# Optimization experiments

Hardware: AMD Instinct MI355X
Metric: run time of the kernel (lower is better)

Reference implementation:

```python
import math
import jax, jax.numpy as jnp
import numpy as np

B_SZ, N_TOK, D_INNER, S_STATE = 4, 1024, 384, 16
DT_MAX = 0.15


def setup_inputs() -> dict:
    key = jax.random.key(0)
    ks = jax.random.split(key, 10)
    dt_init = math.log(math.exp(0.1) - 1.0)  # softplus^-1(0.1)
    x = jax.random.normal(ks[0], (B_SZ, N_TOK, D_INNER), dtype=jnp.float32)
    dt_self_W = jax.random.uniform(ks[1], (D_INNER, D_INNER), minval=-1e-4, maxval=1e-4)
    dt_self_b = jnp.full((D_INNER,), dt_init, dtype=jnp.float32)
    dt_diff_W = jax.random.uniform(ks[2], (D_INNER, D_INNER), minval=-1e-4, maxval=1e-4)
    dt_diff_b = jnp.full((D_INNER,), dt_init, dtype=jnp.float32)
    B_W = jax.random.normal(ks[3], (D_INNER, S_STATE)) / math.sqrt(D_INNER)
    C_real_W = jax.random.normal(ks[4], (D_INNER, S_STATE)) / math.sqrt(D_INNER)
    C_imag_W = jax.random.normal(ks[5], (D_INNER, S_STATE)) / math.sqrt(D_INNER)
    D_param = jnp.ones((D_INNER,), dtype=jnp.float32)
    A_log = jnp.broadcast_to(jnp.log(jnp.arange(1, S_STATE + 1, dtype=jnp.float32))[None, :], (D_INNER, S_STATE))
    lap = jnp.array([[0.0, 1.0, 0.0], [1.0, -4.0, 1.0], [0.0, 1.0, 0.0]], dtype=jnp.float32) * 0.1
    conv_w = jnp.broadcast_to(lap[None, None], (D_INNER, 1, 3, 3)) + 0.01 * jax.random.normal(ks[6], (D_INNER, 1, 3, 3))
    reaction_alpha = 0.01 * jax.random.normal(ks[7], (1, 1, D_INNER, 1))
    reaction_beta = 0.01 * jax.random.normal(ks[8], (1, 1, D_INNER, 1))
    return {
        'x': x, 'dt_self_W': dt_self_W, 'dt_self_b': dt_self_b,
        'dt_diff_W': dt_diff_W, 'dt_diff_b': dt_diff_b,
        'B_W': B_W, 'C_real_W': C_real_W, 'C_imag_W': C_imag_W,
        'D_param': D_param, 'A_log': A_log, 'conv_w': conv_w,
        'reaction_alpha': reaction_alpha, 'reaction_beta': reaction_beta,
        'K_steps': 2,
    }


def _laplacian(h, conv_w, H, W):
    # h: (B, N, D, S) -> depthwise 3x3 conv with replicate pad over the HxW grid
    B, N, D, S = h.shape
    hs = h.transpose(0, 3, 2, 1).reshape(B * S, D, H, W)
    hp = jnp.pad(hs, ((0, 0), (0, 0), (1, 1), (1, 1)), mode='edge')
    lap = jax.lax.conv_general_dilated(
        hp, conv_w, window_strides=(1, 1), padding='VALID',
        feature_group_count=D, dimension_numbers=('NCHW', 'OIHW', 'NCHW'))
    return lap.reshape(B, S, D, N).transpose(0, 3, 2, 1)


def reference(x, dt_self_W, dt_self_b, dt_diff_W, dt_diff_b, B_W, C_real_W,
              C_imag_W, D_param, A_log, conv_w, reaction_alpha, reaction_beta,
              K_steps):
    B, N, D = x.shape
    H = Wg = int(math.sqrt(N))
    A = -jax.nn.softplus(A_log)  # (D, S)
    delta_s = jnp.minimum(jax.nn.softplus(x @ dt_self_W.T + dt_self_b), DT_MAX)[..., None]
    delta_d = jnp.minimum(jax.nn.softplus(x @ dt_diff_W.T + dt_diff_b), DT_MAX)[..., None]
    B_mat = x @ B_W          # (B, N, S)
    C_real = x @ C_real_W    # (B, N, S)
    C_imag = x @ C_imag_W    # (B, N, S)
    mamba_input = jnp.einsum('bnd,bns->bnds', x, B_mat)
    h_real = mamba_input
    h_imag = jnp.zeros_like(h_real)
    dt = 1.0 / K_steps
    A_exp = A[None, None]  # (1,1,D,S)
    for _ in range(K_steps):
        f1_real = delta_s * (A_exp * h_real + mamba_input)
        f1_imag = delta_s * (A_exp * h_imag)
        lap_real = _laplacian(h_real, conv_w, H, Wg)
        lap_imag = _laplacian(h_imag, conv_w, H, Wg)
        f2_real = delta_d * -lap_imag
        f2_imag = delta_d * lap_real
        reaction_scale = reaction_alpha - reaction_beta * (h_real ** 2 + h_imag ** 2)
        h_real = h_real + dt * (f1_real + f2_real + h_real * reaction_scale)
        h_imag = h_imag + dt * (f1_imag + f2_imag + h_imag * reaction_scale)
    y = (jnp.einsum('bnds,bns->bnd', h_real, C_real)
         + jnp.einsum('bnds,bns->bnd', h_imag, C_imag)
         + x * D_param)
    return y
```

## Files before the change

kernel.cpp:

```cpp
#include <hip/hip_runtime.h>
#include <math.h>

#define B_SZ    4
#define N_TOKC  1024
#define D_INNER 384
#define S_STATE 16
#define DT_MAX_V 0.15f
#define PLANE   (B_SZ * N_TOKC)
#define DN      ((size_t)B_SZ * D_INNER * N_TOKC)

typedef __attribute__((ext_vector_type(8))) short bf16x8;
typedef __attribute__((ext_vector_type(4))) float f32x4;

__device__ __forceinline__ float softplusf(float z) {
    return fmaxf(z, 0.f) + log1pf(expf(-fabsf(z)));
}

__device__ __forceinline__ unsigned short f2bf(float f) {
    unsigned u = __float_as_uint(f);
    unsigned r = (u + 0x7FFFu + ((u >> 16) & 1u)) >> 16;
    return (unsigned short)r;
}

__device__ __forceinline__ unsigned packbf(float hr, float hi) {
    return (__float_as_uint(hr) & 0xFFFF0000u) | (__float_as_uint(hi) >> 16);
}

__device__ __forceinline__ size_t frag_off(int T, int kb, int q, int l16) {
    return ((size_t)((T * 12 + kb) * 4 + q)) * 128 + l16 * 8;
}

__device__ __forceinline__ bf16x8 pack8(const float* v) {
    bf16x8 o;
#pragma unroll
    for (int e = 0; e < 8; e++) o[e] = (short)f2bf(v[e]);
    return o;
}

__global__ __launch_bounds__(256) void k_prep(
    const float* __restrict__ x, const float* __restrict__ Ws, const float* __restrict__ Wd,
    const float* __restrict__ BW, const float* __restrict__ CrW, const float* __restrict__ CiW,
    float* __restrict__ x_t, unsigned short* __restrict__ xp,
    unsigned short* __restrict__ Wdtp, unsigned short* __restrict__ Wbcp)
{
    const int t = threadIdx.x;
    const int bx = blockIdx.x;
    if (bx < 1536) {
        __shared__ __align__(16) float tile[32][36];
        const int tok0 = (bx & 127) * 32;
        const int d0   = (bx >> 7) * 32;
        const int b = tok0 >> 10, n0 = tok0 & 1023;
        {
            const int r = t >> 3, c4 = (t & 7) * 4;
            const float4 v = *(const float4*)(x + (size_t)(tok0 + r) * D_INNER + d0 + c4);
            tile[r][c4 + 0] = v.x; tile[r][c4 + 1] = v.y;
            tile[r][c4 + 2] = v.z; tile[r][c4 + 3] = v.w;
        }
        __syncthreads();
        {
            const int dr = t >> 3, n4 = (t & 7) * 4;
            float4 o;
            o.x = tile[n4 + 0][dr]; o.y = tile[n4 + 1][dr];
            o.z = tile[n4 + 2][dr]; o.w = tile[n4 + 3][dr];
            *(float4*)(x_t + ((size_t)(b * D_INNER + d0 + dr)) * N_TOKC + n0 + n4) = o;
        }
        if (t < 128) {
            const int tt = t >> 6, q = (t >> 4) & 3, l16 = t & 15;
            const int row = tt * 16 + l16;
            float v[8];
#pragma unroll
            for (int e = 0; e < 8; e++) v[e] = tile[row][q * 8 + e];
            *(bf16x8*)(xp + frag_off((tok0 >> 4) + tt, d0 >> 5, q, l16)) = pack8(v);
        }
    } else if (bx < 1584) {
        const int vv = bx - 1536;
        const int mat = vv >= 24;
        const int dt16 = mat ? vv - 24 : vv;
        const float* W = mat ? Wd : Ws;
        unsigned short* dst = Wdtp + (size_t)mat * 147456;
#pragma unroll
        for (int it = 0; it < 3; it++) {
            const int item = t + it * 256;
            const int l16 = item & 15, q = (item >> 4) & 3, kb = item >> 6;
            const float* src = W + (size_t)(dt16 * 16 + l16) * D_INNER + kb * 32 + q * 8;
            float v[8];
            const float4 v0 = *(const float4*)(src);
            const float4 v1 = *(const float4*)(src + 4);
            v[0] = v0.x; v[1] = v0.y; v[2] = v0.z; v[3] = v0.w;
            v[4] = v1.x; v[5] = v1.y; v[6] = v1.z; v[7] = v1.w;
            *(bf16x8*)(dst + frag_off(dt16, kb, q, l16)) = pack8(v);
        }
    } else {
        const int m = bx - 1584;
        const float* W2 = (m == 0) ? BW : ((m == 1) ? CrW : CiW);
#pragma unroll
        for (int it = 0; it < 3; it++) {
            const int item = t + it * 256;
            const int l16 = item & 15, q = (item >> 4) & 3, kb = item >> 6;
            float v[8];
#pragma unroll
            for (int e = 0; e < 8; e++)
                v[e] = W2[(size_t)(kb * 32 + q * 8 + e) * S_STATE + l16];
            *(bf16x8*)(Wbcp + (size_t)m * 6144 + frag_off(0, kb, q, l16)) = pack8(v);
        }
    }
}

__global__ __launch_bounds__(256) void k_gemm(
    const unsigned short* __restrict__ xp, const unsigned short* __restrict__ Wdtp,
    const unsigned short* __restrict__ Wbcp,
    const float* __restrict__ bs, const float* __restrict__ bd,
    float* __restrict__ ds_t, float* __restrict__ dd_t,
    float* __restrict__ Bm_t, float* __restrict__ Cr_t, float* __restrict__ Ci_t)
{
    const int wave = threadIdx.x >> 6;
    const int lane = threadIdx.x & 63;
    const int quad = lane >> 4, l16 = lane & 15;

    if (blockIdx.x < 384) {
        const int dbase = (blockIdx.x >> 6) * 64;
        const int tbase = (blockIdx.x & 63) * 64;
        const int wd = (wave & 1) * 32;
        const int wt = (wave >> 1) * 32;
        const int dT0 = (dbase + wd) >> 4;
        const int tT0 = (tbase + wt) >> 4;

        f32x4 acc[2][2][2];
#pragma unroll
        for (int m = 0; m < 2; m++)
#pragma unroll
            for (int i = 0; i < 2; i++)
#pragma unroll
                for (int j = 0; j < 2; j++) acc[m][i][j] = (f32x4)0.f;

#pragma unroll
        for (int kb = 0; kb < 12; kb++) {
            bf16x8 a[2][2], b[2];
#pragma unroll
            for (int m = 0; m < 2; m++)
#pragma unroll
                for (int i = 0; i < 2; i++)
                    a[m][i] = *(const bf16x8*)(Wdtp + (size_t)m * 147456
                                               + frag_off(dT0 + i, kb, quad, l16));
#pragma unroll
            for (int j = 0; j < 2; j++)
                b[j] = *(const bf16x8*)(xp + frag_off(tT0 + j, kb, quad, l16));
#pragma unroll
            for (int m = 0; m < 2; m++)
#pragma unroll
                for (int i = 0; i < 2; i++)
#pragma unroll
                    for (int j = 0; j < 2; j++)
                        acc[m][i][j] = __builtin_amdgcn_mfma_f32_16x16x32_bf16(
                            a[m][i], b[j], acc[m][i][j], 0, 0, 0);
        }

#pragma unroll
        for (int m = 0; m < 2; m++) {
            const float* bias = (m == 0) ? bs : bd;
            float* out = (m == 0) ? ds_t : dd_t;
#pragma unroll
            for (int i = 0; i < 2; i++)
#pragma unroll
                for (int j = 0; j < 2; j++) {
                    const int tok = tbase + wt + j * 16 + l16;
                    const int bb = tok >> 10, n = tok & 1023;
#pragma unroll
                    for (int reg = 0; reg < 4; reg++) {
                        const int d = dbase + wd + i * 16 + quad * 4 + reg;
                        const float v = fminf(softplusf(acc[m][i][j][reg] + bias[d]), DT_MAX_V);
                        out[((size_t)(bb * D_INNER + d)) * N_TOKC + n] = v;
                    }
                }
        }
    } else {
        const int tT = (blockIdx.x - 384) * 4 + wave;
        f32x4 acc[3];
#pragma unroll
        for (int m = 0; m < 3; m++) acc[m] = (f32x4)0.f;

#pragma unroll
        for (int kb = 0; kb < 12; kb++) {
            const bf16x8 b = *(const bf16x8*)(xp + frag_off(tT, kb, quad, l16));
#pragma unroll
            for (int m = 0; m < 3; m++) {
                const bf16x8 a = *(const bf16x8*)(Wbcp + (size_t)m * 6144
                                                  + frag_off(0, kb, quad, l16));
                acc[m] = __builtin_amdgcn_mfma_f32_16x16x32_bf16(a, b, acc[m], 0, 0, 0);
            }
        }

        const int tok = tT * 16 + l16;
#pragma unroll
        for (int m = 0; m < 3; m++) {
            float* plane = (m == 0) ? Bm_t : ((m == 1) ? Cr_t : Ci_t);
#pragma unroll
            for (int reg = 0; reg < 4; reg++) {
                const int s = quad * 4 + reg;
                plane[(size_t)s * PLANE + tok] = acc[m][reg];
            }
        }
    }
}

__global__ __launch_bounds__(256) void k_ssm(
    const float* __restrict__ x_t, const float* __restrict__ conv_w, const float* __restrict__ A_log,
    const float* __restrict__ ralpha, const float* __restrict__ rbeta, const float* __restrict__ Dp,
    const float* __restrict__ ds_t, const float* __restrict__ dd_t,
    const float* __restrict__ Bm_t, const float* __restrict__ Cr_t, const float* __restrict__ Ci_t,
    float* __restrict__ y_part)
{
    const int sg = blockIdx.x;
    const int d  = blockIdx.y;
    const int b  = blockIdx.z;
    const int t  = threadIdx.x;
    const int c  = t & 31;
    const int g  = t >> 5;
    const int r0 = g * 4;

    __shared__ unsigned pl[4][34 * 34];

    float w[9];
#pragma unroll
    for (int i = 0; i < 9; i++) w[i] = conv_w[d * 9 + i];
    const float alpha = ralpha[d];
    const float beta  = rbeta[d];
    const float Dv    = Dp[d];
    float A[4];
#pragma unroll
    for (int s = 0; s < 4; s++) A[s] = -softplusf(A_log[d * S_STATE + sg * 4 + s]);

    const size_t base_dn = ((size_t)(b * D_INNER + d)) * N_TOKC;
    const size_t base_sn = (size_t)b * N_TOKC;

    float xv[4], dsv[4], ddv[4], Bmv[4][4];
    float hr[4][4], hi[4][4];
#pragma unroll
    for (int k = 0; k < 4; k++) {
        const int n = (r0 + k) * 32 + c;
        xv[k]  = x_t [base_dn + n];
        dsv[k] = ds_t[base_dn + n];
        ddv[k] = dd_t[base_dn + n];
#pragma unroll
        for (int s = 0; s < 4; s++) {
            Bmv[k][s] = Bm_t[(size_t)(sg * 4 + s) * PLANE + base_sn + n];
            hr[k][s]  = xv[k] * Bmv[k][s];
        }
    }

    const int wslot = (r0 + 1) * 34 + (c + 1);
    const int rbase = r0 * 34 + c;

#pragma unroll
    for (int s = 0; s < 4; s++) {
#pragma unroll
        for (int k = 0; k < 4; k++)
            pl[s][wslot + k * 34] = __float_as_uint(hr[k][s]);
        if (g == 0) pl[s][c + 1]           = __float_as_uint(hr[0][s]);
        if (g == 7) pl[s][33 * 34 + c + 1] = __float_as_uint(hr[3][s]);
        if (c == 0) {
#pragma unroll
            for (int k = 0; k < 4; k++) pl[s][(r0 + 1 + k) * 34] = __float_as_uint(hr[k][s]);
            if (g == 0) pl[s][0]       = __float_as_uint(hr[0][s]);
            if (g == 7) pl[s][33 * 34] = __float_as_uint(hr[3][s]);
        }
        if (c == 31) {
#pragma unroll
            for (int k = 0; k < 4; k++) pl[s][(r0 + 1 + k) * 34 + 33] = __float_as_uint(hr[k][s]);
            if (g == 0) pl[s][33]           = __float_as_uint(hr[0][s]);
            if (g == 7) pl[s][33 * 34 + 33] = __float_as_uint(hr[3][s]);
        }
    }
    __syncthreads();

    float lr0[4][4];
#pragma unroll
    for (int s = 0; s < 4; s++) {
        float fr[6][3];
#pragma unroll
        for (int rr = 0; rr < 6; rr++)
#pragma unroll
            for (int bb = 0; bb < 3; bb++)
                fr[rr][bb] = __uint_as_float(pl[s][rbase + rr * 34 + bb]);
#pragma unroll
        for (int k = 0; k < 4; k++) {
            float ar = 0.f;
#pragma unroll
            for (int a = 0; a < 3; a++)
#pragma unroll
                for (int bb = 0; bb < 3; bb++)
                    ar = fmaf(w[a * 3 + bb], fr[k + a][bb], ar);
            lr0[k][s] = ar;
        }
    }
    __syncthreads();

#pragma unroll
    for (int k = 0; k < 4; k++)
#pragma unroll
        for (int s = 0; s < 4; s++) {
            const float hrv = hr[k][s];
            const float u   = xv[k] * Bmv[k][s];
            const float f1r = dsv[k] * fmaf(A[s], hrv, u);
            const float rs  = fmaf(-beta, hrv * hrv, alpha);
            hr[k][s] = hrv + 0.5f * (f1r + hrv * rs);
            hi[k][s] = 0.5f * ddv[k] * lr0[k][s];
        }

#pragma unroll
    for (int s = 0; s < 4; s++) {
#pragma unroll
        for (int k = 0; k < 4; k++)
            pl[s][wslot + k * 34] = packbf(hr[k][s], hi[k][s]);
        if (g == 0) pl[s][c + 1]           = packbf(hr[0][s], hi[0][s]);
        if (g == 7) pl[s][33 * 34 + c + 1] = packbf(hr[3][s], hi[3][s]);
        if (c == 0) {
#pragma unroll
            for (int k = 0; k < 4; k++) pl[s][(r0 + 1 + k) * 34] = packbf(hr[k][s], hi[k][s]);
            if (g == 0) pl[s][0]       = packbf(hr[0][s], hi[0][s]);
            if (g == 7) pl[s][33 * 34] = packbf(hr[3][s], hi[3][s]);
        }
        if (c == 31) {
#pragma unroll
            for (int k = 0; k < 4; k++) pl[s][(r0 + 1 + k) * 34 + 33] = packbf(hr[k][s], hi[k][s]);
            if (g == 0) pl[s][33]           = packbf(hr[0][s], hi[0][s]);
            if (g == 7) pl[s][33 * 34 + 33] = packbf(hr[3][s], hi[3][s]);
        }
    }
    __syncthreads();

    float lr1[4][4], li1[4][4];
#pragma unroll
    for (int s = 0; s < 4; s++) {
        float fr[6][3], fi[6][3];
#pragma unroll
        for (int rr = 0; rr < 6; rr++)
#pragma unroll
            for (int bb = 0; bb < 3; bb++) {
                const unsigned u = pl[s][rbase + rr * 34 + bb];
                fr[rr][bb] = __uint_as_float(u & 0xFFFF0000u);
                fi[rr][bb] = __uint_as_float(u << 16);
            }
#pragma unroll
        for (int k = 0; k < 4; k++) {
            float ar = 0.f, ai = 0.f;
#pragma unroll
            for (int a = 0; a < 3; a++)
#pragma unroll
                for (int bb = 0; bb < 3; bb++) {
                    const float wt = w[a * 3 + bb];
                    ar = fmaf(wt, fr[k + a][bb], ar);
                    ai = fmaf(wt, fi[k + a][bb], ai);
                }
            lr1[k][s] = ar; li1[k][s] = ai;
        }
    }

#pragma unroll
    for (int k = 0; k < 4; k++)
#pragma unroll
        for (int s = 0; s < 4; s++) {
            const float hrv = hr[k][s], hiv = hi[k][s];
            const float u   = xv[k] * Bmv[k][s];
            const float f1r = dsv[k] * fmaf(A[s], hrv, u);
            const float f1i = dsv[k] * (A[s] * hiv);
            const float f2r = -ddv[k] * li1[k][s];
            const float f2i =  ddv[k] * lr1[k][s];
            const float q   = fmaf(hrv, hrv, hiv * hiv);
            const float rs  = fmaf(-beta, q, alpha);
            hr[k][s] = hrv + 0.5f * (f1r + f2r + hrv * rs);
            hi[k][s] = hiv + 0.5f * (f1i + f2i + hiv * rs);
        }

#pragma unroll
    for (int k = 0; k < 4; k++) {
        const int n = (r0 + k) * 32 + c;
        float yp = 0.f;
#pragma unroll
        for (int s = 0; s < 4; s++) {
            const size_t po = (size_t)(sg * 4 + s) * PLANE + base_sn + n;
            yp = fmaf(hr[k][s], Cr_t[po], yp);
            yp = fmaf(hi[k][s], Ci_t[po], yp);
        }
        if (sg == 0) yp = fmaf(xv[k], Dv, yp);
        y_part[((size_t)((sg * B_SZ + b) * D_INNER + d)) * N_TOKC + n] = yp;
    }
}

__global__ __launch_bounds__(256) void k_reduce(
    const float* __restrict__ y_part, float* __restrict__ y)
{
    const int d0 = blockIdx.x * 32;
    const int n0 = blockIdx.y * 32;
    const int b  = blockIdx.z;
    const int t  = threadIdx.x;
    __shared__ __align__(16) float tile[32][36];

    const int dr = t >> 3, nc4 = (t & 7) * 4;
    float4 acc = make_float4(0.f, 0.f, 0.f, 0.f);
#pragma unroll
    for (int sg = 0; sg < 4; sg++) {
        const float4 v = *(const float4*)(y_part
            + ((size_t)((sg * B_SZ + b) * D_INNER + d0 + dr)) * N_TOKC + n0 + nc4);
        acc.x += v.x; acc.y += v.y; acc.z += v.z; acc.w += v.w;
    }
    *(float4*)&tile[dr][nc4] = acc;
    __syncthreads();

    const int nr = t >> 3, dc4 = (t & 7) * 4;
    float4 o;
    o.x = tile[dc4 + 0][nr];
    o.y = tile[dc4 + 1][nr];
    o.z = tile[dc4 + 2][nr];
    o.w = tile[dc4 + 3][nr];
    *(float4*)(y + ((size_t)(b * N_TOKC + n0 + nr)) * D_INNER + d0 + dc4) = o;
}

extern "C" void kernel_launch(void* const* d_in, const int* in_sizes, int n_in,
                              void* d_out, int out_size, void* d_ws, size_t ws_size,
                              hipStream_t stream)
{
    const float* x    = (const float*)d_in[0];
    const float* Ws   = (const float*)d_in[1];
    const float* bsb  = (const float*)d_in[2];
    const float* Wd   = (const float*)d_in[3];
    const float* bdb  = (const float*)d_in[4];
    const float* BW   = (const float*)d_in[5];
    const float* CrW  = (const float*)d_in[6];
    const float* CiW  = (const float*)d_in[7];
    const float* Dp   = (const float*)d_in[8];
    const float* Alog = (const float*)d_in[9];
    const float* cw   = (const float*)d_in[10];
    const float* ra   = (const float*)d_in[11];
    const float* rb   = (const float*)d_in[12];
    float* y = (float*)d_out;

    float* ws     = (float*)d_ws;
    float* ds_t   = ws;
    float* dd_t   = ds_t + DN;
    float* x_t    = dd_t + DN;
    float* Bm_t   = x_t + DN;
    float* Cr_t   = Bm_t + (size_t)S_STATE * PLANE;
    float* Ci_t   = Cr_t + (size_t)S_STATE * PLANE;
    float* y_part = Ci_t + (size_t)S_STATE * PLANE;

    unsigned short* xp   = (unsigned short*)y_part;
    unsigned short* Wdtp = xp + (size_t)256 * 12 * 4 * 128;
    unsigned short* Wbcp = Wdtp + (size_t)2 * 147456;

    k_prep<<<dim3(1587), 256, 0, stream>>>(x, Ws, Wd, BW, CrW, CiW, x_t, xp, Wdtp, Wbcp);
    k_gemm<<<dim3(448), 256, 0, stream>>>(xp, Wdtp, Wbcp, bsb, bdb,
                                          ds_t, dd_t, Bm_t, Cr_t, Ci_t);
    k_ssm<<<dim3(4, D_INNER, B_SZ), 256, 0, stream>>>(x_t, cw, Alog, ra, rb, Dp,
                                                      ds_t, dd_t, Bm_t, Cr_t, Ci_t, y_part);
    k_reduce<<<dim3(12, 32, 4), 256, 0, stream>>>(y_part, y);
}
```

Baseline: 175.9 us.

## Use packed fp16 math for Laplacian stencil and prefetch MFMA operands

The stencil state in shared memory is now stored as packed fp16 pairs instead of truncated bf16, and the 3x3 Laplacian is accumulated with packed half2 FMAs, roughly halving the stencil ALU work. The dt projection GEMM loop gains register double-buffering of the next k-block's fragments with partial unrolling, and the B/C projection loop is no longer unrolled. The fp16 accumulation keeps fewer exponent bits than fp32 and may add rounding error or overflow risk. The unroll changes trade instruction scheduling freedom for lower register pressure.

```diff
diff --git a/kernel.cpp b/kernel.cpp
--- a/kernel.cpp
+++ b/kernel.cpp
@@ -1,4 +1,5 @@
 #include <hip/hip_runtime.h>
+#include <hip/hip_fp16.h>
 #include <math.h>
 
 #define B_SZ    4
@@ -22,8 +23,12 @@
     return (unsigned short)r;
 }
 
-__device__ __forceinline__ unsigned packbf(float hr, float hi) {
-    return (__float_as_uint(hr) & 0xFFFF0000u) | (__float_as_uint(hi) >> 16);
+__device__ __forceinline__ unsigned packh2(float hr, float hi) {
+    __half2 h = __floats2half2_rn(hr, hi);
+    union { __half2 h; unsigned u; } c; c.h = h; return c.u;
+}
+__device__ __forceinline__ __half2 uph2(unsigned u) {
+    union { unsigned u; __half2 h; } c; c.u = u; return c.h;
 }
 
 __device__ __forceinline__ size_t frag_off(int T, int kb, int q, int l16) {
@@ -133,18 +138,31 @@
 #pragma unroll
                 for (int j = 0; j < 2; j++) acc[m][i][j] = (f32x4)0.f;
 
-#pragma unroll
+        bf16x8 a0[2][2], b0[2];
+#pragma unroll
+        for (int m = 0; m < 2; m++)
+#pragma unroll
+            for (int i = 0; i < 2; i++)
+                a0[m][i] = *(const bf16x8*)(Wdtp + (size_t)m * 147456
+                                            + frag_off(dT0 + i, 0, quad, l16));
+#pragma unroll
+        for (int j = 0; j < 2; j++)
+            b0[j] = *(const bf16x8*)(xp + frag_off(tT0 + j, 0, quad, l16));
+
+#pragma unroll 2
         for (int kb = 0; kb < 12; kb++) {
-            bf16x8 a[2][2], b[2];
+            bf16x8 a1[2][2], b1[2];
+            const int kn = (kb < 11) ? kb + 1 : 11;
 #pragma unroll
             for (int m = 0; m < 2; m++)
 #pragma unroll
                 for (int i = 0; i < 2; i++)
-                    a[m][i] = *(const bf16x8*)(Wdtp + (size_t)m * 147456
-                                               + frag_off(dT0 + i, kb, quad, l16));
+                    a1[m][i] = *(const bf16x8*)(Wdtp + (size_t)m * 147456
+                                                + frag_off(dT0 + i, kn, quad, l16));
 #pragma unroll
             for (int j = 0; j < 2; j++)
-                b[j] = *(const bf16x8*)(xp + frag_off(tT0 + j, kb, quad, l16));
+                b1[j] = *(const bf16x8*)(xp + frag_off(tT0 + j, kn, quad, l16));
+
 #pragma unroll
             for (int m = 0; m < 2; m++)
 #pragma unroll
@@ -152,7 +170,14 @@
 #pragma unroll
                     for (int j = 0; j < 2; j++)
                         acc[m][i][j] = __builtin_amdgcn_mfma_f32_16x16x32_bf16(
-                            a[m][i], b[j], acc[m][i][j], 0, 0, 0);
+                            a0[m][i], b0[j], acc[m][i][j], 0, 0, 0);
+
+#pragma unroll
+            for (int m = 0; m < 2; m++)
+#pragma unroll
+                for (int i = 0; i < 2; i++) a0[m][i] = a1[m][i];
+#pragma unroll
+            for (int j = 0; j < 2; j++) b0[j] = b1[j];
         }
 
 #pragma unroll
@@ -179,7 +204,7 @@
 #pragma unroll
         for (int m = 0; m < 3; m++) acc[m] = (f32x4)0.f;
 
-#pragma unroll
+#pragma unroll 1
         for (int kb = 0; kb < 12; kb++) {
             const bf16x8 b = *(const bf16x8*)(xp + frag_off(tT, kb, quad, l16));
 #pragma unroll
@@ -223,6 +248,9 @@
     float w[9];
 #pragma unroll
     for (int i = 0; i < 9; i++) w[i] = conv_w[d * 9 + i];
+    __half2 wh[9];
+#pragma unroll
+    for (int i = 0; i < 9; i++) wh[i] = __float2half2_rn(w[i]);
     const float alpha = ralpha[d];
     const float beta  = rbeta[d];
     const float Dv    = Dp[d];
@@ -311,20 +339,20 @@
     for (int s = 0; s < 4; s++) {
 #pragma unroll
         for (int k = 0; k < 4; k++)
-            pl[s][wslot + k * 34] = packbf(hr[k][s], hi[k][s]);
-        if (g == 0) pl[s][c + 1]           = packbf(hr[0][s], hi[0][s]);
-        if (g == 7) pl[s][33 * 34 + c + 1] = packbf(hr[3][s], hi[3][s]);
+            pl[s][wslot + k * 34] = packh2(hr[k][s], hi[k][s]);
+        if (g == 0) pl[s][c + 1]           = packh2(hr[0][s], hi[0][s]);
+        if (g == 7) pl[s][33 * 34 + c + 1] = packh2(hr[3][s], hi[3][s]);
         if (c == 0) {
 #pragma unroll
-            for (int k = 0; k < 4; k++) pl[s][(r0 + 1 + k) * 34] = packbf(hr[k][s], hi[k][s]);
-            if (g == 0) pl[s][0]       = packbf(hr[0][s], hi[0][s]);
-            if (g == 7) pl[s][33 * 34] = packbf(hr[3][s], hi[3][s]);
+            for (int k = 0; k < 4; k++) pl[s][(r0 + 1 + k) * 34] = packh2(hr[k][s], hi[k][s]);
+            if (g == 0) pl[s][0]       = packh2(hr[0][s], hi[0][s]);
+            if (g == 7) pl[s][33 * 34] = packh2(hr[3][s], hi[3][s]);
         }
         if (c == 31) {
 #pragma unroll
-            for (int k = 0; k < 4; k++) pl[s][(r0 + 1 + k) * 34 + 33] = packbf(hr[k][s], hi[k][s]);
-            if (g == 0) pl[s][33]           = packbf(hr[0][s], hi[0][s]);
-            if (g == 7) pl[s][33 * 34 + 33] = packbf(hr[3][s], hi[3][s]);
+            for (int k = 0; k < 4; k++) pl[s][(r0 + 1 + k) * 34 + 33] = packh2(hr[k][s], hi[k][s]);
+            if (g == 0) pl[s][33]           = packh2(hr[0][s], hi[0][s]);
+            if (g == 7) pl[s][33 * 34 + 33] = packh2(hr[3][s], hi[3][s]);
         }
     }
     __syncthreads();
@@ -332,27 +360,22 @@
     float lr1[4][4], li1[4][4];
 #pragma unroll
     for (int s = 0; s < 4; s++) {
-        float fr[6][3], fi[6][3];
+        __half2 f2[6][3];
 #pragma unroll
         for (int rr = 0; rr < 6; rr++)
 #pragma unroll
-            for (int bb = 0; bb < 3; bb++) {
-                const unsigned u = pl[s][rbase + rr * 34 + bb];
-                fr[rr][bb] = __uint_as_float(u & 0xFFFF0000u);
-                fi[rr][bb] = __uint_as_float(u << 16);
-            }
+            for (int bb = 0; bb < 3; bb++)
+                f2[rr][bb] = uph2(pl[s][rbase + rr * 34 + bb]);
 #pragma unroll
         for (int k = 0; k < 4; k++) {
-            float ar = 0.f, ai = 0.f;
+            __half2 ac = __float2half2_rn(0.f);
 #pragma unroll
             for (int a = 0; a < 3; a++)
 #pragma unroll
-                for (int bb = 0; bb < 3; bb++) {
-                    const float wt = w[a * 3 + bb];
-                    ar = fmaf(wt, fr[k + a][bb], ar);
-                    ai = fmaf(wt, fi[k + a][bb], ai);
-                }
-            lr1[k][s] = ar; li1[k][s] = ai;
+                for (int bb = 0; bb < 3; bb++)
+                    ac = __hfma2(wh[a * 3 + bb], f2[k + a][bb], ac);
+            lr1[k][s] = __low2float(ac);
+            li1[k][s] = __high2float(ac);
         }
     }
 
```

Result: no change. 173.9 us (-1.1%).
